# Kernel optimization log

Measured on AMD Instinct MI355X. Metric: run time of the kernel, lower is better.

Reference implementation:

```python
import jax, jax.numpy as jnp
import numpy as np

N_HEAD = 16


def setup_inputs() -> dict:
    key = jax.random.key(0)
    ks = jax.random.split(key, 9)
    B, T, C = 4, 2048, 1024
    s = 1.0 / np.sqrt(C)
    x = jax.random.normal(ks[0], (B, T, C), dtype=jnp.float32)
    Wq = jax.random.normal(ks[1], (C, C), dtype=jnp.float32) * s
    bq = jnp.zeros((C,), dtype=jnp.float32)
    Wk = jax.random.normal(ks[2], (C, C), dtype=jnp.float32) * s
    bk = jnp.zeros((C,), dtype=jnp.float32)
    Wv = jax.random.normal(ks[3], (C, C), dtype=jnp.float32) * s
    bv = jnp.zeros((C,), dtype=jnp.float32)
    Wp = jax.random.normal(ks[4], (C, C), dtype=jnp.float32) * s
    bp = jnp.zeros((C,), dtype=jnp.float32)
    return {"x": x, "Wq": Wq, "bq": bq, "Wk": Wk, "bk": bk,
            "Wv": Wv, "bv": bv, "Wp": Wp, "bp": bp}


def reference(x, Wq, bq, Wk, bk, Wv, bv, Wp, bp):
    B, T, C = x.shape
    H = N_HEAD
    D = C // H
    # QKV projections, then split heads: [B, T, C] -> [B, H, T, D]
    def split_heads(t):
        return t.reshape(B, T, H, D).transpose(0, 2, 1, 3)
    q = split_heads(x @ Wq.T + bq)
    k = split_heads(x @ Wk.T + bk)
    v = split_heads(x @ Wv.T + bv)
    # NOTE: original code applies NO causal mask despite the class name.
    att = jnp.einsum('bhtd,bhsd->bhts', q, k) * (1.0 / jnp.sqrt(jnp.float32(D)))
    att = jax.nn.softmax(att, axis=-1)
    y = jnp.einsum('bhts,bhsd->bhtd', att, v)  # [B, H, T, D]
    y = y.transpose(0, 2, 1, 3).reshape(B, T, C)
    return y @ Wp.T + bp
```

## Files before the change

### kernel.cpp

```cpp
#include <hip/hip_runtime.h>
#include <hip/hip_bf16.h>

typedef float  f32x4   __attribute__((ext_vector_type(4)));
typedef short  bf16x8  __attribute__((ext_vector_type(8)));

__device__ __forceinline__ ushort f2b(float f) {
  union { float f; unsigned u; } x; x.f = f;
  unsigned r = x.u + 0x7fffu + ((x.u >> 16) & 1u);
  return (ushort)(r >> 16);
}

__device__ __forceinline__ unsigned pk2(float lo, float hi) {
  __hip_bfloat162 t = __float22bfloat162_rn(make_float2(lo, hi));
  union { __hip_bfloat162 b; unsigned u; } c; c.b = t; return c.u;
}

__device__ __forceinline__ f32x4 fzero() {
  f32x4 z; z[0] = 0.f; z[1] = 0.f; z[2] = 0.f; z[3] = 0.f; return z;
}

__device__ __forceinline__ void gld_lds16(const ushort* g, ushort* l) {
  __builtin_amdgcn_global_load_lds(g, l, 16, 0, 0);
}

__device__ __forceinline__ int vperm_s(int j64) {
  return (j64 & 0x23) | ((j64 & 0x0C) << 1) | ((j64 & 0x10) >> 2);
}

__global__ __launch_bounds__(256) void f2bf_kernel(const float* __restrict__ in,
                                                   ushort* __restrict__ out, int n4) {
  int idx = blockIdx.x * 256 + threadIdx.x;
  int stride = gridDim.x * 256;
  for (int i = idx; i < n4; i += stride) {
    float4 v = reinterpret_cast<const float4*>(in)[i];
    ushort4 o;
    o.x = f2b(v.x); o.y = f2b(v.y); o.z = f2b(v.z); o.w = f2b(v.w);
    reinterpret_cast<ushort4*>(out)[i] = o;
  }
}

__global__ __launch_bounds__(256) void f2bf_w4(
    const float* __restrict__ w0, const float* __restrict__ w1,
    const float* __restrict__ w2, const float* __restrict__ w3,
    ushort* __restrict__ out, int n4) {
  const float* src = (blockIdx.y == 0) ? w0 : (blockIdx.y == 1) ? w1
                   : (blockIdx.y == 2) ? w2 : w3;
  ushort* dst = out + (size_t)blockIdx.y * (size_t)n4 * 4;
  int idx = blockIdx.x * 256 + threadIdx.x;
  int stride = gridDim.x * 256;
  for (int i = idx; i < n4; i += stride) {
    float4 v = reinterpret_cast<const float4*>(src)[i];
    ushort4 o;
    o.x = f2b(v.x); o.y = f2b(v.y); o.z = f2b(v.z); o.w = f2b(v.w);
    reinterpret_cast<ushort4*>(dst)[i] = o;
  }
}

__global__ __launch_bounds__(256) void gemm_bt(
    const ushort* __restrict__ A, const ushort* __restrict__ B,
    const float* __restrict__ bias, float* __restrict__ Cf, ushort* __restrict__ Cb,
    int M, int N, int K, float scale) {
  __shared__ ushort As[128 * 32];
  __shared__ ushort Bs[128 * 32];
  const int tid = threadIdx.x, lane = tid & 63, wave = tid >> 6;
  const int wr = (wave >> 1) << 6, wc = (wave & 1) << 6;
  const int fr = lane & 15, fk8 = (lane >> 4) << 3;

  const size_t rowA = (size_t)blockIdx.y * 128;
  const size_t rowB = (size_t)blockIdx.x * 128;
  const ushort* Ag = A + rowA * K;
  const ushort* Bg = B + rowB * K;

  const int c0 = tid, c1 = tid + 256;
  const size_t a0 = (size_t)(c0 >> 2) * K + (size_t)((c0 & 3) << 3);
  const size_t a1 = (size_t)(c1 >> 2) * K + (size_t)((c1 & 3) << 3);

  f32x4 acc[4][4];
#pragma unroll
  for (int m = 0; m < 4; ++m)
#pragma unroll
    for (int n = 0; n < 4; ++n) acc[m][n] = fzero();

  for (int k0 = 0; k0 < K; k0 += 32) {
    __syncthreads();
    gld_lds16(Ag + a0 + k0, &As[wave * 512]);
    gld_lds16(Ag + a1 + k0, &As[2048 + wave * 512]);
    gld_lds16(Bg + a0 + k0, &Bs[wave * 512]);
    gld_lds16(Bg + a1 + k0, &Bs[2048 + wave * 512]);
    asm volatile("s_waitcnt vmcnt(0)" ::: "memory");
    __syncthreads();

    bf16x8 af[4], bfv[4];
#pragma unroll
    for (int m = 0; m < 4; ++m)
      af[m] = *reinterpret_cast<const bf16x8*>(&As[(wr + m * 16 + fr) * 32 + fk8]);
#pragma unroll
    for (int n = 0; n < 4; ++n)
      bfv[n] = *reinterpret_cast<const bf16x8*>(&Bs[(wc + n * 16 + fr) * 32 + fk8]);
#pragma unroll
    for (int m = 0; m < 4; ++m)
#pragma unroll
      for (int n = 0; n < 4; ++n)
        acc[m][n] = __builtin_amdgcn_mfma_f32_16x16x32_bf16(af[m], bfv[n], acc[m][n], 0, 0, 0);
  }

  const int orow = (lane >> 4) << 2;
#pragma unroll
  for (int m = 0; m < 4; ++m) {
#pragma unroll
    for (int n = 0; n < 4; ++n) {
      size_t gc = rowB + wc + n * 16 + fr;
      float bv = bias[gc];
#pragma unroll
      for (int r = 0; r < 4; ++r) {
        size_t gr = rowA + wr + m * 16 + orow + r;
        float v = (acc[m][n][r] + bv) * scale;
        if (Cf) Cf[gr * N + gc] = v;
        else    Cb[gr * N + gc] = f2b(v);
      }
    }
  }
}

__global__ __launch_bounds__(256) void gemm_qkv(
    const ushort* __restrict__ A, const ushort* __restrict__ Bw,
    const float* __restrict__ bq, const float* __restrict__ bk, const float* __restrict__ bv,
    ushort* __restrict__ Qb, ushort* __restrict__ Kb, ushort* __restrict__ VbT,
    float qscale) {
  __shared__ ushort As[128 * 32];
  __shared__ ushort Bs[128 * 32];
  const int tid = threadIdx.x, lane = tid & 63, wave = tid >> 6;
  const int wr = (wave >> 1) << 6, wc = (wave & 1) << 6;
  const int fr = lane & 15, fk8 = (lane >> 4) << 3;
  const int K = 1024;

  const size_t rowA = (size_t)blockIdx.y * 128;
  const size_t rowB = (size_t)blockIdx.x * 128;
  const ushort* Ag = A + rowA * K;
  const ushort* Bg = Bw + rowB * K;

  const int c0 = tid, c1 = tid + 256;
  const size_t a0 = (size_t)(c0 >> 2) * K + (size_t)((c0 & 3) << 3);
  const size_t a1 = (size_t)(c1 >> 2) * K + (size_t)((c1 & 3) << 3);

  f32x4 acc[4][4];
#pragma unroll
  for (int m = 0; m < 4; ++m)
#pragma unroll
    for (int n = 0; n < 4; ++n) acc[m][n] = fzero();

  for (int k0 = 0; k0 < K; k0 += 32) {
    __syncthreads();
    gld_lds16(Ag + a0 + k0, &As[wave * 512]);
    gld_lds16(Ag + a1 + k0, &As[2048 + wave * 512]);
    gld_lds16(Bg + a0 + k0, &Bs[wave * 512]);
    gld_lds16(Bg + a1 + k0, &Bs[2048 + wave * 512]);
    asm volatile("s_waitcnt vmcnt(0)" ::: "memory");
    __syncthreads();

    bf16x8 af[4], bfv[4];
#pragma unroll
    for (int m = 0; m < 4; ++m)
      af[m] = *reinterpret_cast<const bf16x8*>(&As[(wr + m * 16 + fr) * 32 + fk8]);
#pragma unroll
    for (int n = 0; n < 4; ++n)
      bfv[n] = *reinterpret_cast<const bf16x8*>(&Bs[(wc + n * 16 + fr) * 32 + fk8]);
#pragma unroll
    for (int m = 0; m < 4; ++m)
#pragma unroll
      for (int n = 0; n < 4; ++n)
        acc[m][n] = __builtin_amdgcn_mfma_f32_16x16x32_bf16(af[m], bfv[n], acc[m][n], 0, 0, 0);
  }

  const int stripe  = blockIdx.x >> 3;
  const int colbase = (blockIdx.x & 7) * 128;
  const int orow = (lane >> 4) << 2;
#pragma unroll
  for (int m = 0; m < 4; ++m) {
#pragma unroll
    for (int n = 0; n < 4; ++n) {
      const int gcl = colbase + wc + n * 16 + fr;
      if (stripe == 0) {
        const float bb_ = bq[gcl];
#pragma unroll
        for (int r = 0; r < 4; ++r) {
          size_t gr = rowA + wr + m * 16 + orow + r;
          Qb[gr * 1024 + gcl] = f2b((acc[m][n][r] + bb_) * qscale);
        }
      } else if (stripe == 1) {
        const float bb_ = bk[gcl];
#pragma unroll
        for (int r = 0; r < 4; ++r) {
          size_t gr = rowA + wr + m * 16 + orow + r;
          Kb[gr * 1024 + gcl] = f2b(acc[m][n][r] + bb_);
        }
      } else {
        const float bb_ = bv[gcl];
#pragma unroll
        for (int r = 0; r < 4; ++r) {
          int tt = (int)rowA + wr + m * 16 + orow + r;
          int b = tt >> 11, t = tt & 2047;
          size_t idx = (size_t)b * 2097152 + (size_t)gcl * 2048
                     + (size_t)((t & ~63) + vperm_s(t & 63));
          VbT[idx] = f2b(acc[m][n][r] + bb_);
        }
      }
    }
  }
}

__global__ __launch_bounds__(512, 4) void attn_kernel(
    const ushort* __restrict__ Qb, const ushort* __restrict__ Kb,
    const ushort* __restrict__ VbT, ushort* __restrict__ Yb) {
  __shared__ ushort lds[24576];
  const int tid = threadIdx.x, lane = tid & 63, wave = tid >> 6;
  const int fr = lane & 15, g = lane >> 4, fk8 = g << 3;
  const int bb = blockIdx.y >> 4, hh = blockIdx.y & 15;
  const size_t rowbase = (size_t)bb * 2048;
  const int cbase = hh * 64;
  const ushort* Kg  = Kb  + rowbase * 1024 + cbase;
  const ushort* VgT = VbT + (size_t)bb * 2097152 + (size_t)cbase * 2048;

  const int qrow = blockIdx.x * 128 + wave * 16 + fr;
  const ushort* qptr = &Qb[(rowbase + qrow) * 1024 + cbase];
  const bf16x8 qf0 = *reinterpret_cast<const bf16x8*>(qptr + fk8);
  const bf16x8 qf1 = *reinterpret_cast<const bf16x8*>(qptr + 32 + fk8);

  const int rS = tid >> 3;
  const int wS = (tid & 7) ^ (rS & 7);
  const ushort* sKp = Kg  + (size_t)rS * 1024 + (wS << 3);
  const ushort* sVp = VgT + (size_t)rS * 2048 + (wS << 3);
  const int wofs = wave * 512;

  const int e0 = (g ^ (fr & 7)) << 3;
  const int e1 = ((4 + g) ^ (fr & 7)) << 3;
  const ushort* lpA = &lds[fr * 64 + e0];
  const ushort* lpB = &lds[fr * 64 + e1];

  f32x4 yacc[4];
#pragma unroll
  for (int nb = 0; nb < 4; ++nb) yacc[nb] = fzero();
  f32x4 psum4 = fzero();

#define LD8(P) (*reinterpret_cast<const bf16x8*>(P))
#define MF16(A, B, C) __builtin_amdgcn_mfma_f32_16x16x32_bf16(A, B, C, 0, 0, 0)

  gld_lds16(sKp, &lds[wofs]);         gld_lds16(sVp, &lds[12288 + wofs]);   sKp += 65536; sVp += 64;
  gld_lds16(sKp, &lds[4096 + wofs]);  gld_lds16(sVp, &lds[16384 + wofs]);   sKp += 65536; sVp += 64;
  asm volatile("s_waitcnt vmcnt(2)" ::: "memory");
  __builtin_amdgcn_s_barrier();
  __builtin_amdgcn_sched_barrier(0);

#define TILE(BUF, DOPF, VMASM) do {                                              \
    if (DOPF) {                                                                  \
      gld_lds16(sKp, &lds[(((BUF) + 2) % 3) * 4096 + wofs]);                     \
      gld_lds16(sVp, &lds[12288 + (((BUF) + 2) % 3) * 4096 + wofs]);             \
      sKp += 65536; sVp += 64;                                                   \
    }                                                                            \
    f32x4 sT[4];                                                                 \
    _Pragma("unroll")                                                            \
    for (int jb = 0; jb < 4; ++jb) {                                             \
      bf16x8 kf0 = LD8(lpA + (BUF) * 4096 + jb * 1024);                          \
      bf16x8 kf1 = LD8(lpB + (BUF) * 4096 + jb * 1024);                          \
      f32x4 z = fzero();                                                         \
      __builtin_amdgcn_s_setprio(1);                                             \
      z = MF16(kf0, qf0, z);                                                     \
      z = MF16(kf1, qf1, z);                                                     \
      __builtin_amdgcn_s_setprio(0);                                             \
      sT[jb] = z;                                                                \
    }                                                                            \
    _Pragma("unroll")                                                            \
    for (int jb = 0; jb < 4; ++jb)                                               \
      _Pragma("unroll")                                                          \
      for (int r = 0; r < 4; ++r) sT[jb][r] = __builtin_exp2f(sT[jb][r]);        \
    _Pragma("unroll")                                                            \
    for (int r = 0; r < 4; ++r)                                                  \
      psum4[r] += (sT[0][r] + sT[1][r]) + (sT[2][r] + sT[3][r]);                 \
    union { bf16x8 v; unsigned u[4]; } pa0, pa1;                                 \
    pa0.u[0] = pk2(sT[0][0], sT[0][1]); pa0.u[1] = pk2(sT[0][2], sT[0][3]);      \
    pa0.u[2] = pk2(sT[1][0], sT[1][1]); pa0.u[3] = pk2(sT[1][2], sT[1][3]);      \
    pa1.u[0] = pk2(sT[2][0], sT[2][1]); pa1.u[1] = pk2(sT[2][2], sT[2][3]);      \
    pa1.u[2] = pk2(sT[3][0], sT[3][1]); pa1.u[3] = pk2(sT[3][2], sT[3][3]);      \
    _Pragma("unroll")                                                            \
    for (int nb = 0; nb < 4; ++nb) {                                             \
      bf16x8 vf0 = LD8(lpA + 12288 + (BUF) * 4096 + nb * 1024);                  \
      bf16x8 vf1 = LD8(lpB + 12288 + (BUF) * 4096 + nb * 1024);                  \
      __builtin_amdgcn_s_setprio(1);                                             \
      yacc[nb] = MF16(vf0, pa0.v, yacc[nb]);                                     \
      yacc[nb] = MF16(vf1, pa1.v, yacc[nb]);                                     \
      __builtin_amdgcn_s_setprio(0);                                             \
    }                                                                            \
    asm volatile(VMASM ::: "memory");                                            \
    __builtin_amdgcn_s_barrier();                                                \
    __builtin_amdgcn_sched_barrier(0);                                           \
  } while (0)

  for (int tb = 0; tb < 30; tb += 3) {
    TILE(0, 1, "s_waitcnt vmcnt(2)");
    TILE(1, 1, "s_waitcnt vmcnt(2)");
    TILE(2, 1, "s_waitcnt vmcnt(2)");
  }
  TILE(0, 0, "s_waitcnt vmcnt(0)");
  TILE(1, 0, "s_waitcnt vmcnt(0)");
#undef TILE
#undef MF16
#undef LD8

  float psum = (psum4[0] + psum4[1]) + (psum4[2] + psum4[3]);
  psum += __shfl_xor(psum, 16);
  psum += __shfl_xor(psum, 32);
  const float linv = 1.0f / psum;
  ushort* yrow = &Yb[(rowbase + qrow) * 1024 + cbase];
#pragma unroll
  for (int nb = 0; nb < 4; ++nb) {
    ushort4 o;
    o.x = f2b(yacc[nb][0] * linv);
    o.y = f2b(yacc[nb][1] * linv);
    o.z = f2b(yacc[nb][2] * linv);
    o.w = f2b(yacc[nb][3] * linv);
    *reinterpret_cast<ushort4*>(yrow + nb * 16 + (g << 2)) = o;
  }
}

extern "C" void kernel_launch(void* const* d_in, const int* in_sizes, int n_in,
                              void* d_out, int out_size, void* d_ws, size_t ws_size,
                              hipStream_t stream) {
  const float* x  = (const float*)d_in[0];
  const float* Wq = (const float*)d_in[1];
  const float* bq = (const float*)d_in[2];
  const float* Wk = (const float*)d_in[3];
  const float* bk = (const float*)d_in[4];
  const float* Wv = (const float*)d_in[5];
  const float* bv = (const float*)d_in[6];
  const float* Wp = (const float*)d_in[7];
  const float* bp = (const float*)d_in[8];
  float* out = (float*)d_out;

  const int M = 8192, C = 1024;
  const size_t MC = (size_t)M * C, CC = (size_t)C * C;
  const size_t need = (MC * 5 + CC * 4) * sizeof(ushort);
  if (ws_size < need) return;

  ushort* xb  = (ushort*)d_ws;
  ushort* wqb = xb + MC;
  ushort* wpb = wqb + 3 * CC;
  ushort* Qb  = wpb + CC;
  ushort* Kb  = Qb + MC;
  ushort* VbT = Kb + MC;
  ushort* Yb  = VbT + MC;

  f2bf_kernel<<<2048, 256, 0, stream>>>(x, xb, (int)(MC / 4));
  f2bf_w4<<<dim3(256, 4), 256, 0, stream>>>(Wq, Wk, Wv, Wp, wqb, (int)(CC / 4));

  const float QSCALE = 0.18033688011112042f;
  gemm_qkv<<<dim3(24, 64), 256, 0, stream>>>(xb, wqb, bq, bk, bv, Qb, Kb, VbT, QSCALE);

  attn_kernel<<<dim3(16, 64), 512, 0, stream>>>(Qb, Kb, VbT, Yb);

  gemm_bt<<<dim3(8, 64), 256, 0, stream>>>(Yb, wpb, bp, out, nullptr, M, C, C, 1.0f);
}
```

Before: 238.2 us.

## Process two query row-blocks per wave in attention to reuse K/V fragments

```diff
diff --git a/kernel.cpp b/kernel.cpp
--- a/kernel.cpp
+++ b/kernel.cpp
@@ -10,9 +10,10 @@
   return (ushort)(r >> 16);
 }
 
-__device__ __forceinline__ unsigned pk2(float lo, float hi) {
-  __hip_bfloat162 t = __float22bfloat162_rn(make_float2(lo, hi));
-  union { __hip_bfloat162 b; unsigned u; } c; c.b = t; return c.u;
+__device__ __forceinline__ unsigned pkr(float lo, float hi) {
+  unsigned lu = __float_as_uint(lo) + 0x8000u;
+  unsigned hu = __float_as_uint(hi) + 0x8000u;
+  return __builtin_amdgcn_perm(hu, lu, 0x07060302u);
 }
 
 __device__ __forceinline__ f32x4 fzero() {
@@ -196,20 +197,22 @@
         }
       } else {
         const float bb_ = bv[gcl];
-#pragma unroll
-        for (int r = 0; r < 4; ++r) {
-          int tt = (int)rowA + wr + m * 16 + orow + r;
-          int b = tt >> 11, t = tt & 2047;
-          size_t idx = (size_t)b * 2097152 + (size_t)gcl * 2048
-                     + (size_t)((t & ~63) + vperm_s(t & 63));
-          VbT[idx] = f2b(acc[m][n][r] + bb_);
-        }
+        int tt0 = (int)rowA + wr + m * 16 + orow;
+        int b = tt0 >> 11, t = tt0 & 2047;
+        size_t idx0 = (size_t)b * 2097152 + (size_t)gcl * 2048
+                    + (size_t)((t & ~63) + vperm_s(t & 63));
+        ushort4 o;
+        o.x = f2b(acc[m][n][0] + bb_);
+        o.y = f2b(acc[m][n][1] + bb_);
+        o.z = f2b(acc[m][n][2] + bb_);
+        o.w = f2b(acc[m][n][3] + bb_);
+        *reinterpret_cast<ushort4*>(&VbT[idx0]) = o;
       }
     }
   }
 }
 
-__global__ __launch_bounds__(512, 4) void attn_kernel(
+__global__ __launch_bounds__(512, 2) void attn_kernel(
     const ushort* __restrict__ Qb, const ushort* __restrict__ Kb,
     const ushort* __restrict__ VbT, ushort* __restrict__ Yb) {
   __shared__ ushort lds[24576];
@@ -221,10 +224,13 @@
   const ushort* Kg  = Kb  + rowbase * 1024 + cbase;
   const ushort* VgT = VbT + (size_t)bb * 2097152 + (size_t)cbase * 2048;
 
-  const int qrow = blockIdx.x * 128 + wave * 16 + fr;
-  const ushort* qptr = &Qb[(rowbase + qrow) * 1024 + cbase];
-  const bf16x8 qf0 = *reinterpret_cast<const bf16x8*>(qptr + fk8);
-  const bf16x8 qf1 = *reinterpret_cast<const bf16x8*>(qptr + 32 + fk8);
+  const int qbase = blockIdx.x * 256 + wave * 32;
+  const ushort* qpA = &Qb[(rowbase + qbase + fr) * 1024 + cbase];
+  const ushort* qpB = &Qb[(rowbase + qbase + 16 + fr) * 1024 + cbase];
+  const bf16x8 qfA0 = *reinterpret_cast<const bf16x8*>(qpA + fk8);
+  const bf16x8 qfA1 = *reinterpret_cast<const bf16x8*>(qpA + 32 + fk8);
+  const bf16x8 qfB0 = *reinterpret_cast<const bf16x8*>(qpB + fk8);
+  const bf16x8 qfB1 = *reinterpret_cast<const bf16x8*>(qpB + 32 + fk8);
 
   const int rS = tid >> 3;
   const int wS = (tid & 7) ^ (rS & 7);
@@ -237,10 +243,10 @@
   const ushort* lpA = &lds[fr * 64 + e0];
   const ushort* lpB = &lds[fr * 64 + e1];
 
-  f32x4 yacc[4];
-#pragma unroll
-  for (int nb = 0; nb < 4; ++nb) yacc[nb] = fzero();
-  f32x4 psum4 = fzero();
+  f32x4 yA[4], yB[4];
+#pragma unroll
+  for (int nb = 0; nb < 4; ++nb) { yA[nb] = fzero(); yB[nb] = fzero(); }
+  f32x4 psA = fzero(), psB = fzero();
 
 #define LD8(P) (*reinterpret_cast<const bf16x8*>(P))
 #define MF16(A, B, C) __builtin_amdgcn_mfma_f32_16x16x32_bf16(A, B, C, 0, 0, 0)
@@ -257,37 +263,50 @@
       gld_lds16(sVp, &lds[12288 + (((BUF) + 2) % 3) * 4096 + wofs]);             \
       sKp += 65536; sVp += 64;                                                   \
     }                                                                            \
-    f32x4 sT[4];                                                                 \
+    f32x4 sTA[4], sTB[4];                                                        \
     _Pragma("unroll")                                                            \
     for (int jb = 0; jb < 4; ++jb) {                                             \
       bf16x8 kf0 = LD8(lpA + (BUF) * 4096 + jb * 1024);                          \
       bf16x8 kf1 = LD8(lpB + (BUF) * 4096 + jb * 1024);                          \
-      f32x4 z = fzero();                                                         \
+      f32x4 zA = fzero(), zB = fzero();                                          \
       __builtin_amdgcn_s_setprio(1);                                             \
-      z = MF16(kf0, qf0, z);                                                     \
-      z = MF16(kf1, qf1, z);                                                     \
+      zA = MF16(kf0, qfA0, zA);                                                  \
+      zB = MF16(kf0, qfB0, zB);                                                  \
+      zA = MF16(kf1, qfA1, zA);                                                  \
+      zB = MF16(kf1, qfB1, zB);                                                  \
       __builtin_amdgcn_s_setprio(0);                                             \
-      sT[jb] = z;                                                                \
+      sTA[jb] = zA; sTB[jb] = zB;                                                \
     }                                                                            \
     _Pragma("unroll")                                                            \
     for (int jb = 0; jb < 4; ++jb)                                               \
       _Pragma("unroll")                                                          \
-      for (int r = 0; r < 4; ++r) sT[jb][r] = __builtin_exp2f(sT[jb][r]);        \
+      for (int r = 0; r < 4; ++r) {                                              \
+        sTA[jb][r] = __builtin_exp2f(sTA[jb][r]);                                \
+        sTB[jb][r] = __builtin_exp2f(sTB[jb][r]);                                \
+      }                                                                          \
     _Pragma("unroll")                                                            \
-    for (int r = 0; r < 4; ++r)                                                  \
-      psum4[r] += (sT[0][r] + sT[1][r]) + (sT[2][r] + sT[3][r]);                 \
-    union { bf16x8 v; unsigned u[4]; } pa0, pa1;                                 \
-    pa0.u[0] = pk2(sT[0][0], sT[0][1]); pa0.u[1] = pk2(sT[0][2], sT[0][3]);      \
-    pa0.u[2] = pk2(sT[1][0], sT[1][1]); pa0.u[3] = pk2(sT[1][2], sT[1][3]);      \
-    pa1.u[0] = pk2(sT[2][0], sT[2][1]); pa1.u[1] = pk2(sT[2][2], sT[2][3]);      \
-    pa1.u[2] = pk2(sT[3][0], sT[3][1]); pa1.u[3] = pk2(sT[3][2], sT[3][3]);      \
+    for (int r = 0; r < 4; ++r) {                                                \
+      psA[r] += (sTA[0][r] + sTA[1][r]) + (sTA[2][r] + sTA[3][r]);               \
+      psB[r] += (sTB[0][r] + sTB[1][r]) + (sTB[2][r] + sTB[3][r]);               \
+    }                                                                            \
+    union { bf16x8 v; unsigned u[4]; } paA0, paA1, paB0, paB1;                   \
+    paA0.u[0] = pkr(sTA[0][0], sTA[0][1]); paA0.u[1] = pkr(sTA[0][2], sTA[0][3]);\
+    paA0.u[2] = pkr(sTA[1][0], sTA[1][1]); paA0.u[3] = pkr(sTA[1][2], sTA[1][3]);\
+    paA1.u[0] = pkr(sTA[2][0], sTA[2][1]); paA1.u[1] = pkr(sTA[2][2], sTA[2][3]);\
+    paA1.u[2] = pkr(sTA[3][0], sTA[3][1]); paA1.u[3] = pkr(sTA[3][2], sTA[3][3]);\
+    paB0.u[0] = pkr(sTB[0][0], sTB[0][1]); paB0.u[1] = pkr(sTB[0][2], sTB[0][3]);\
+    paB0.u[2] = pkr(sTB[1][0], sTB[1][1]); paB0.u[3] = pkr(sTB[1][2], sTB[1][3]);\
+    paB1.u[0] = pkr(sTB[2][0], sTB[2][1]); paB1.u[1] = pkr(sTB[2][2], sTB[2][3]);\
+    paB1.u[2] = pkr(sTB[3][0], sTB[3][1]); paB1.u[3] = pkr(sTB[3][2], sTB[3][3]);\
     _Pragma("unroll")                                                            \
     for (int nb = 0; nb < 4; ++nb) {                                             \
       bf16x8 vf0 = LD8(lpA + 12288 + (BUF) * 4096 + nb * 1024);                  \
       bf16x8 vf1 = LD8(lpB + 12288 + (BUF) * 4096 + nb * 1024);                  \
       __builtin_amdgcn_s_setprio(1);                                             \
-      yacc[nb] = MF16(vf0, pa0.v, yacc[nb]);                                     \
-      yacc[nb] = MF16(vf1, pa1.v, yacc[nb]);                                     \
+      yA[nb] = MF16(vf0, paA0.v, yA[nb]);                                        \
+      yB[nb] = MF16(vf0, paB0.v, yB[nb]);                                        \
+      yA[nb] = MF16(vf1, paA1.v, yA[nb]);                                        \
+      yB[nb] = MF16(vf1, paB1.v, yB[nb]);                                        \
       __builtin_amdgcn_s_setprio(0);                                             \
     }                                                                            \
     asm volatile(VMASM ::: "memory");                                            \
@@ -306,19 +325,25 @@
 #undef MF16
 #undef LD8
 
-  float psum = (psum4[0] + psum4[1]) + (psum4[2] + psum4[3]);
-  psum += __shfl_xor(psum, 16);
-  psum += __shfl_xor(psum, 32);
-  const float linv = 1.0f / psum;
-  ushort* yrow = &Yb[(rowbase + qrow) * 1024 + cbase];
+  float pa_ = (psA[0] + psA[1]) + (psA[2] + psA[3]);
+  pa_ += __shfl_xor(pa_, 16);
+  pa_ += __shfl_xor(pa_, 32);
+  float pb_ = (psB[0] + psB[1]) + (psB[2] + psB[3]);
+  pb_ += __shfl_xor(pb_, 16);
+  pb_ += __shfl_xor(pb_, 32);
+  const float liA = 1.0f / pa_;
+  const float liB = 1.0f / pb_;
+  ushort* yrA = &Yb[(rowbase + qbase + fr) * 1024 + cbase];
+  ushort* yrB = &Yb[(rowbase + qbase + 16 + fr) * 1024 + cbase];
 #pragma unroll
   for (int nb = 0; nb < 4; ++nb) {
-    ushort4 o;
-    o.x = f2b(yacc[nb][0] * linv);
-    o.y = f2b(yacc[nb][1] * linv);
-    o.z = f2b(yacc[nb][2] * linv);
-    o.w = f2b(yacc[nb][3] * linv);
-    *reinterpret_cast<ushort4*>(yrow + nb * 16 + (g << 2)) = o;
+    ushort4 oA, oB;
+    oA.x = f2b(yA[nb][0] * liA); oA.y = f2b(yA[nb][1] * liA);
+    oA.z = f2b(yA[nb][2] * liA); oA.w = f2b(yA[nb][3] * liA);
+    oB.x = f2b(yB[nb][0] * liB); oB.y = f2b(yB[nb][1] * liB);
+    oB.z = f2b(yB[nb][2] * liB); oB.w = f2b(yB[nb][3] * liB);
+    *reinterpret_cast<ushort4*>(yrA + nb * 16 + (g << 2)) = oA;
+    *reinterpret_cast<ushort4*>(yrB + nb * 16 + (g << 2)) = oB;
   }
 }
 
@@ -355,7 +380,7 @@
   const float QSCALE = 0.18033688011112042f;
   gemm_qkv<<<dim3(24, 64), 256, 0, stream>>>(xb, wqb, bq, bk, bv, Qb, Kb, VbT, QSCALE);
 
-  attn_kernel<<<dim3(16, 64), 512, 0, stream>>>(Qb, Kb, VbT, Yb);
+  attn_kernel<<<dim3(8, 64), 512, 0, stream>>>(Qb, Kb, VbT, Yb);
 
   gemm_bt<<<dim3(8, 64), 256, 0, stream>>>(Yb, wpb, bp, out, nullptr, M, C, C, 1.0f);
 }
```

Measured after the change: 242.6 us. No clear change (+1.9%).
